# Performance work log

Hardware: AMD Instinct MI355X
Metric: run time of the kernel (lower is better)

## Reference

```python
import jax, jax.numpy as jnp
import numpy as np

N = 50000      # nodes
E = 500000     # edges (before self-loops)
IN = 128       # input feature dim
HID = 64       # hidden per head
HEADS = 8
OUT = 40       # classes
NEG_SLOPE = 0.2  # PyG GATConv default


def setup_inputs() -> dict:
    key = jax.random.key(0)
    ks = jax.random.split(key, 10)
    s = 0.05
    return {
        "x": jax.random.normal(ks[0], (N, IN), jnp.float32),
        "edge_index": jax.random.randint(ks[1], (2, E), 0, N, dtype=jnp.int32),
        "W1": jax.random.normal(ks[2], (IN, HEADS * HID), jnp.float32) * s,
        "a1_src": jax.random.normal(ks[3], (HEADS, HID), jnp.float32) * s,
        "a1_dst": jax.random.normal(ks[4], (HEADS, HID), jnp.float32) * s,
        "b1": jnp.zeros((HEADS * HID,), jnp.float32),
        "W2": jax.random.normal(ks[5], (HEADS * HID, OUT), jnp.float32) * s,
        "a2_src": jax.random.normal(ks[6], (1, OUT), jnp.float32) * s,
        "a2_dst": jax.random.normal(ks[7], (1, OUT), jnp.float32) * s,
        "b2": jnp.zeros((OUT,), jnp.float32),
    }


def gat_layer(x, src, dst, W, a_src, a_dst, b, heads, ch, concat):
    n = x.shape[0]
    h = (x @ W).reshape(n, heads, ch)                    # [N,H,C]
    e_src = jnp.einsum('nhc,hc->nh', h, a_src)           # [N,H]
    e_dst = jnp.einsum('nhc,hc->nh', h, a_dst)
    logits = jax.nn.leaky_relu(e_src[src] + e_dst[dst], NEG_SLOPE)  # [E,H]
    # segment softmax over incoming edges of each dst node
    m = jax.ops.segment_max(logits, dst, num_segments=n)
    p = jnp.exp(logits - m[dst])
    z = jax.ops.segment_sum(p, dst, num_segments=n)
    alpha = p / (z[dst] + 1e-16)                         # [E,H]
    out = jax.ops.segment_sum(h[src] * alpha[:, :, None], dst, num_segments=n)  # [N,H,C]
    out = out.reshape(n, heads * ch) if concat else out.mean(axis=1)
    return out + b


def reference(x, edge_index, W1, a1_src, a1_dst, b1, W2, a2_src, a2_dst, b2):
    loops = jnp.arange(N, dtype=edge_index.dtype)
    src = jnp.concatenate([edge_index[0], loops])        # add self-loops (PyG default)
    dst = jnp.concatenate([edge_index[1], loops])
    h = jax.nn.relu(gat_layer(x, src, dst, W1, a1_src, a1_dst, b1, HEADS, HID, True))
    h = gat_layer(h, src, dst, W2, a2_src, a2_dst, b2, 1, OUT, False)
    return jax.nn.log_softmax(h, axis=1)
```

## Files before the change

kernel.cpp:

```cpp
#include <hip/hip_runtime.h>
#include <math.h>

#define N_NODES 50000
#define E_EDGES 500000
#define E_TOT   550000
#define IN_DIM  128
#define HID     64
#define HEADS   8
#define HC      512
#define OUT_DIM 40
#define NEG_SLOPE 0.2f

__device__ __forceinline__ float leaky(float v){ return v > 0.f ? v : NEG_SLOPE * v; }


__global__ void k_hist(const int* __restrict__ ei, int* __restrict__ counts){
    int i = blockIdx.x * 256 + threadIdx.x;
    if (i < E_EDGES){
        atomicAdd(&counts[ei[E_EDGES + i]], 1);
    } else if (i < E_TOT){
        atomicAdd(&counts[i - E_EDGES], 1);
    }
}

__global__ void k_scanA(const int* __restrict__ counts, int* __restrict__ offsets,
                        int* __restrict__ blockSums){
    __shared__ int sh[1024];
    int b = blockIdx.x, t = threadIdx.x;
    int i = b * 1024 + t;
    int v = (i < N_NODES) ? counts[i] : 0;
    sh[t] = v; __syncthreads();
    for (int off = 1; off < 1024; off <<= 1){
        int add = (t >= off) ? sh[t - off] : 0;
        __syncthreads();
        sh[t] += add;
        __syncthreads();
    }
    if (i < N_NODES) offsets[i + 1] = sh[t];
    if (t == 1023) blockSums[b] = sh[t];
}

__global__ void k_scanB(int* __restrict__ blockSums, int nb){
    if (threadIdx.x == 0 && blockIdx.x == 0){
        int run = 0;
        for (int b = 0; b < nb; b++){ int v = blockSums[b]; blockSums[b] = run; run += v; }
    }
}

__global__ void k_scanC(const int* __restrict__ counts, int* __restrict__ offsets,
                        const int* __restrict__ blockSums, int* __restrict__ cursor){
    int b = blockIdx.x, t = threadIdx.x;
    int i = b * 1024 + t;
    if (i < N_NODES){
        int v = offsets[i + 1] + blockSums[b];
        offsets[i + 1] = v;
        cursor[i] = v - counts[i];
    }
    if (i == 0) offsets[0] = 0;
}

__global__ void k_scatter(const int* __restrict__ ei, int* __restrict__ cursor,
                          int* __restrict__ sortedSrc){
    int i = blockIdx.x * 256 + threadIdx.x;
    if (i < E_EDGES){
        int d = ei[E_EDGES + i];
        int pos = atomicAdd(&cursor[d], 1);
        sortedSrc[pos] = ei[i];
    } else if (i < E_TOT){
        int n = i - E_EDGES;
        int pos = atomicAdd(&cursor[n], 1);
        sortedSrc[pos] = n;
    }
}


__global__ __launch_bounds__(256) void k_gemm1e1(const float* __restrict__ x,
                                                 const float* __restrict__ W1,
                                                 const float* __restrict__ a1s,
                                                 const float* __restrict__ a1d,
                                                 float* __restrict__ h1,
                                                 float* __restrict__ e1s,
                                                 float* __restrict__ e1d){
    __shared__ float xs[16 * IN_DIM];
    const int t = threadIdx.x;
    const int row0 = blockIdx.x * 16;
    const float4* xg = (const float4*)(x + (size_t)row0 * IN_DIM);
    float4* xsv = (float4*)xs;
    xsv[t] = xg[t];
    xsv[t + 256] = xg[t + 256];
    __syncthreads();

    const int ct = t & 127;
    const int rg = t >> 7;
    float4 acc[8];
    #pragma unroll
    for (int r = 0; r < 8; r++) acc[r] = make_float4(0.f, 0.f, 0.f, 0.f);

    const float4* Wv = (const float4*)W1;
    for (int kb = 0; kb < IN_DIM; kb += 4){
        float4 w0 = Wv[(size_t)(kb + 0) * 128 + ct];
        float4 w1 = Wv[(size_t)(kb + 1) * 128 + ct];
        float4 w2 = Wv[(size_t)(kb + 2) * 128 + ct];
        float4 w3 = Wv[(size_t)(kb + 3) * 128 + ct];
        #pragma unroll
        for (int r = 0; r < 8; r++){
            float4 xv = *(const float4*)&xs[(rg * 8 + r) * IN_DIM + kb];
            acc[r].x = fmaf(xv.x, w0.x, acc[r].x); acc[r].y = fmaf(xv.x, w0.y, acc[r].y);
            acc[r].z = fmaf(xv.x, w0.z, acc[r].z); acc[r].w = fmaf(xv.x, w0.w, acc[r].w);
            acc[r].x = fmaf(xv.y, w1.x, acc[r].x); acc[r].y = fmaf(xv.y, w1.y, acc[r].y);
            acc[r].z = fmaf(xv.y, w1.z, acc[r].z); acc[r].w = fmaf(xv.y, w1.w, acc[r].w);
            acc[r].x = fmaf(xv.z, w2.x, acc[r].x); acc[r].y = fmaf(xv.z, w2.y, acc[r].y);
            acc[r].z = fmaf(xv.z, w2.z, acc[r].z); acc[r].w = fmaf(xv.z, w2.w, acc[r].w);
            acc[r].x = fmaf(xv.w, w3.x, acc[r].x); acc[r].y = fmaf(xv.w, w3.y, acc[r].y);
            acc[r].z = fmaf(xv.w, w3.z, acc[r].z); acc[r].w = fmaf(xv.w, w3.w, acc[r].w);
        }
    }

    const float4 as4 = ((const float4*)a1s)[ct];
    const float4 ad4 = ((const float4*)a1d)[ct];
    float4* h1v = (float4*)h1;
    float ps[8], pd[8];
    #pragma unroll
    for (int r = 0; r < 8; r++){
        int row = row0 + rg * 8 + r;
        h1v[(size_t)row * 128 + ct] = acc[r];
        ps[r] = acc[r].x * as4.x + acc[r].y * as4.y + acc[r].z * as4.z + acc[r].w * as4.w;
        pd[r] = acc[r].x * ad4.x + acc[r].y * ad4.y + acc[r].z * ad4.z + acc[r].w * ad4.w;
    }
    #pragma unroll
    for (int off = 1; off < 16; off <<= 1){
        #pragma unroll
        for (int r = 0; r < 8; r++){
            ps[r] += __shfl_xor(ps[r], off, 64);
            pd[r] += __shfl_xor(pd[r], off, 64);
        }
    }
    if ((t & 15) == 0){
        int h = (ct >> 4) & 7;
        #pragma unroll
        for (int r = 0; r < 8; r++){
            int row = row0 + rg * 8 + r;
            e1s[(size_t)row * HEADS + h] = ps[r];
            e1d[(size_t)row * HEADS + h] = pd[r];
        }
    }
}


__global__ __launch_bounds__(256) void k_agg1(const float* __restrict__ h1,
                                              const float* __restrict__ e1s,
                                              const float* __restrict__ e1d,
                                              const int* __restrict__ offsets,
                                              const int* __restrict__ sortedSrc,
                                              const float* __restrict__ b1,
                                              float* __restrict__ hmid){
    const int lane = threadIdx.x & 63;
    const int d = blockIdx.x * 4 + (threadIdx.x >> 6);
    if (d >= N_NODES) return;
    const int beg = offsets[d], end = offsets[d + 1];
    const int cnt = end - beg;
    const int h = lane >> 3;
    const int c0 = lane * 8;
    const float ed = e1d[(size_t)d * HEADS + h];

    float4 acc0 = make_float4(0.f,0.f,0.f,0.f), acc1 = make_float4(0.f,0.f,0.f,0.f);
    float z = 0.f;

    int s1 = 0, s2 = 0;
    float eA = 0.f; float4 hA0, hA1;
    {
        int s0 = sortedSrc[beg];
        eA = e1s[(size_t)s0 * HEADS + h];
        const float4* hp = (const float4*)(h1 + (size_t)s0 * HC + c0);
        hA0 = hp[0]; hA1 = hp[1];
        if (cnt > 1) s1 = sortedSrc[beg + 1];
    }
    for (int e = 0; e < cnt; ++e){
        if (e + 2 < cnt) s2 = sortedSrc[beg + e + 2];
        float eB = 0.f; float4 hB0, hB1;
        if (e + 1 < cnt){
            eB = e1s[(size_t)s1 * HEADS + h];
            const float4* hp = (const float4*)(h1 + (size_t)s1 * HC + c0);
            hB0 = hp[0]; hB1 = hp[1];
        }
        float w = __expf(leaky(eA + ed));
        z += w;
        acc0.x = fmaf(w, hA0.x, acc0.x); acc0.y = fmaf(w, hA0.y, acc0.y);
        acc0.z = fmaf(w, hA0.z, acc0.z); acc0.w = fmaf(w, hA0.w, acc0.w);
        acc1.x = fmaf(w, hA1.x, acc1.x); acc1.y = fmaf(w, hA1.y, acc1.y);
        acc1.z = fmaf(w, hA1.z, acc1.z); acc1.w = fmaf(w, hA1.w, acc1.w);
        eA = eB; hA0 = hB0; hA1 = hB1; s1 = s2;
    }

    const float inv = 1.f / (z + 1e-16f);
    const float4 bv0 = ((const float4*)b1)[lane * 2];
    const float4 bv1 = ((const float4*)b1)[lane * 2 + 1];
    float4 o0, o1;
    o0.x = fmaxf(fmaf(acc0.x, inv, bv0.x), 0.f);
    o0.y = fmaxf(fmaf(acc0.y, inv, bv0.y), 0.f);
    o0.z = fmaxf(fmaf(acc0.z, inv, bv0.z), 0.f);
    o0.w = fmaxf(fmaf(acc0.w, inv, bv0.w), 0.f);
    o1.x = fmaxf(fmaf(acc1.x, inv, bv1.x), 0.f);
    o1.y = fmaxf(fmaf(acc1.y, inv, bv1.y), 0.f);
    o1.z = fmaxf(fmaf(acc1.z, inv, bv1.z), 0.f);
    o1.w = fmaxf(fmaf(acc1.w, inv, bv1.w), 0.f);
    float4* op = (float4*)(hmid + (size_t)d * HC + c0);
    op[0] = o0; op[1] = o1;
}


__global__ __launch_bounds__(256) void k_gemm2e2(const float* __restrict__ hmid,
                                                 const float* __restrict__ W2,
                                                 const float* __restrict__ a2s,
                                                 const float* __restrict__ a2d,
                                                 float* __restrict__ h2,
                                                 float* __restrict__ e2s,
                                                 float* __restrict__ e2d){
    __shared__ float hs[64][64];
    __shared__ float ws[64 * OUT_DIM];
    const int t = threadIdx.x;
    const int row0 = blockIdx.x * 64;
    const int col = t & 63;
    const int rbase = t >> 6;
    float acc[16];
    #pragma unroll
    for (int i = 0; i < 16; i++) acc[i] = 0.f;

    for (int kb = 0; kb < HC; kb += 64){
        for (int i = t; i < 64 * 64; i += 256){
            int r = i >> 6, k = i & 63;
            int gr = row0 + r;
            hs[r][k] = (gr < N_NODES) ? hmid[(size_t)gr * HC + kb + k] : 0.f;
        }
        for (int i = t; i < 64 * OUT_DIM; i += 256){
            int k = i / OUT_DIM, j = i - k * OUT_DIM;
            ws[i] = W2[(size_t)(kb + k) * OUT_DIM + j];
        }
        __syncthreads();
        if (col < OUT_DIM){
            for (int k = 0; k < 64; k++){
                float w = ws[k * OUT_DIM + col];
                #pragma unroll
                for (int i = 0; i < 16; i++)
                    acc[i] = fmaf(hs[rbase + 4 * i][k], w, acc[i]);
            }
        }
        __syncthreads();
    }

    const float as = (col < OUT_DIM) ? a2s[col] : 0.f;
    const float ad = (col < OUT_DIM) ? a2d[col] : 0.f;
    #pragma unroll
    for (int i = 0; i < 16; i++){
        int r = row0 + rbase + 4 * i;
        bool ok = (col < OUT_DIM) && (r < N_NODES);
        float v = ok ? acc[i] : 0.f;
        if (ok) h2[(size_t)r * OUT_DIM + col] = v;
        float pvs = v * as, pvd = v * ad;
        #pragma unroll
        for (int off = 32; off > 0; off >>= 1){
            pvs += __shfl_xor(pvs, off, 64);
            pvd += __shfl_xor(pvd, off, 64);
        }
        if (col == 0 && r < N_NODES){ e2s[r] = pvs; e2d[r] = pvd; }
    }
}


__global__ __launch_bounds__(256) void k_agg2(const float* __restrict__ h2,
                                              const float* __restrict__ e2s,
                                              const float* __restrict__ e2d,
                                              const int* __restrict__ offsets,
                                              const int* __restrict__ sortedSrc,
                                              const float* __restrict__ b2,
                                              float* __restrict__ out){
    const int lane = threadIdx.x & 63;
    const int d = blockIdx.x * 4 + (threadIdx.x >> 6);
    if (d >= N_NODES) return;
    const int beg = offsets[d], end = offsets[d + 1];
    const int cnt = end - beg;
    const float ed = e2d[d];
    const bool act = (lane < OUT_DIM);

    float acc = 0.f, z = 0.f;
    int s1 = 0, s2 = 0;
    float eA = 0.f, hA = 0.f;
    {
        int s0 = sortedSrc[beg];
        eA = e2s[s0];
        if (act) hA = h2[(size_t)s0 * OUT_DIM + lane];
        if (cnt > 1) s1 = sortedSrc[beg + 1];
    }
    for (int e = 0; e < cnt; ++e){
        if (e + 2 < cnt) s2 = sortedSrc[beg + e + 2];
        float eB = 0.f, hB = 0.f;
        if (e + 1 < cnt){
            eB = e2s[s1];
            if (act) hB = h2[(size_t)s1 * OUT_DIM + lane];
        }
        float w = __expf(leaky(eA + ed));
        z += w;
        acc = fmaf(w, hA, acc);
        eA = eB; hA = hB; s1 = s2;
    }

    float o = acc / (z + 1e-16f) + (act ? b2[lane] : 0.f);
    float ov = act ? o : -INFINITY;
    float vmax = ov;
    #pragma unroll
    for (int off = 32; off > 0; off >>= 1) vmax = fmaxf(vmax, __shfl_xor(vmax, off, 64));
    float se = act ? __expf(o - vmax) : 0.f;
    #pragma unroll
    for (int off = 32; off > 0; off >>= 1) se += __shfl_xor(se, off, 64);
    if (act) out[(size_t)d * OUT_DIM + lane] = o - vmax - __logf(se);
}


extern "C" void kernel_launch(void* const* d_in, const int* in_sizes, int n_in,
                              void* d_out, int out_size, void* d_ws, size_t ws_size,
                              hipStream_t stream){
    const float* x   = (const float*)d_in[0];
    const int*   ei  = (const int*)  d_in[1];
    const float* W1  = (const float*)d_in[2];
    const float* a1s = (const float*)d_in[3];
    const float* a1d = (const float*)d_in[4];
    const float* b1  = (const float*)d_in[5];
    const float* W2  = (const float*)d_in[6];
    const float* a2s = (const float*)d_in[7];
    const float* a2d = (const float*)d_in[8];
    const float* b2  = (const float*)d_in[9];
    float* out = (float*)d_out;

    char* ws = (char*)d_ws;
    size_t off = 0;
    auto alloc = [&](size_t bytes) -> char* {
        off = (off + 255) & ~(size_t)255;
        char* p = ws + off;
        off += bytes;
        return p;
    };

    float* h1      = (float*)alloc((size_t)N_NODES * HC * 4);
    float* hmid    = (float*)alloc((size_t)N_NODES * HC * 4);
    float* h2      = (float*)alloc((size_t)N_NODES * OUT_DIM * 4);
    float* e1s     = (float*)alloc((size_t)N_NODES * HEADS * 4);
    float* e1d     = (float*)alloc((size_t)N_NODES * HEADS * 4);
    float* e2s     = (float*)alloc((size_t)N_NODES * 4);
    float* e2d     = (float*)alloc((size_t)N_NODES * 4);
    int* counts    = (int*)alloc((size_t)N_NODES * 4);
    int* offsets   = (int*)alloc((size_t)(N_NODES + 1) * 4);
    int* cursor    = (int*)alloc((size_t)N_NODES * 4);
    int* blockSums = (int*)alloc(64 * 4);
    int* sortedSrc = (int*)alloc((size_t)E_TOT * 4);

    const int nb = (N_NODES + 1023) / 1024;

    hipMemsetAsync(counts, 0, (size_t)N_NODES * 4, stream);
    k_hist   <<<(E_TOT + 255) / 256, 256, 0, stream>>>(ei, counts);
    k_scanA  <<<nb, 1024, 0, stream>>>(counts, offsets, blockSums);
    k_scanB  <<<1, 64, 0, stream>>>(blockSums, nb);
    k_scanC  <<<nb, 1024, 0, stream>>>(counts, offsets, blockSums, cursor);
    k_scatter<<<(E_TOT + 255) / 256, 256, 0, stream>>>(ei, cursor, sortedSrc);

    k_gemm1e1<<<N_NODES / 16, 256, 0, stream>>>(x, W1, a1s, a1d, h1, e1s, e1d);
    k_agg1   <<<(N_NODES + 3) / 4, 256, 0, stream>>>(h1, e1s, e1d, offsets, sortedSrc, b1, hmid);

    k_gemm2e2<<<(N_NODES + 63) / 64, 256, 0, stream>>>(hmid, W2, a2s, a2d, h2, e2s, e2d);
    k_agg2   <<<(N_NODES + 3) / 4, 256, 0, stream>>>(h2, e2s, e2d, offsets, sortedSrc, b2, out);
}
```

Baseline: 644.1 us.

## Register-block the second-layer GEMM with 4x5 per-thread tiles

The layer-2 GEMM kernel is rewritten so each thread computes a 4-row by 5-column output tile instead of 16 rows of one column. The old version left 24 of every 64 lanes idle. Each block now covers 128 rows with a 32-wide K tile, loads hmid with float4, and stores padded, transposed W2 in shared memory so the inner loop can read float2 values. The attention-score reduction shrinks to a 3-step shuffle across 8 lanes. This raises arithmetic intensity and removes idle lanes, at the cost of more registers and possible LDS bank conflicts.

```diff
diff --git a/kernel.cpp b/kernel.cpp
--- a/kernel.cpp
+++ b/kernel.cpp
@@ -216,53 +216,71 @@
                                                  float* __restrict__ h2,
                                                  float* __restrict__ e2s,
                                                  float* __restrict__ e2d){
-    __shared__ float hs[64][64];
-    __shared__ float ws[64 * OUT_DIM];
+    __shared__ float hs[128][34];
+    __shared__ float ws[OUT_DIM][34];
     const int t = threadIdx.x;
-    const int row0 = blockIdx.x * 64;
-    const int col = t & 63;
-    const int rbase = t >> 6;
-    float acc[16];
-    #pragma unroll
-    for (int i = 0; i < 16; i++) acc[i] = 0.f;
-
-    for (int kb = 0; kb < HC; kb += 64){
-        for (int i = t; i < 64 * 64; i += 256){
-            int r = i >> 6, k = i & 63;
+    const int row0 = blockIdx.x * 128;
+    const int tc = t & 7;
+    const int tr = t >> 3;
+
+    float acc[4][5];
+    #pragma unroll
+    for (int i = 0; i < 4; i++)
+        #pragma unroll
+        for (int j = 0; j < 5; j++) acc[i][j] = 0.f;
+
+    for (int kb = 0; kb < HC; kb += 32){
+        #pragma unroll
+        for (int p = 0; p < 4; p++){
+            int q = t + 256 * p;
+            int r = q >> 3, k4 = (q & 7) * 4;
             int gr = row0 + r;
-            hs[r][k] = (gr < N_NODES) ? hmid[(size_t)gr * HC + kb + k] : 0.f;
-        }
-        for (int i = t; i < 64 * OUT_DIM; i += 256){
+            float4 v = (gr < N_NODES) ? *(const float4*)&hmid[(size_t)gr * HC + kb + k4]
+                                      : make_float4(0.f, 0.f, 0.f, 0.f);
+            *(float2*)&hs[r][k4]     = make_float2(v.x, v.y);
+            *(float2*)&hs[r][k4 + 2] = make_float2(v.z, v.w);
+        }
+        for (int i = t; i < 32 * OUT_DIM; i += 256){
             int k = i / OUT_DIM, j = i - k * OUT_DIM;
-            ws[i] = W2[(size_t)(kb + k) * OUT_DIM + j];
+            ws[j][k] = W2[(size_t)(kb + k) * OUT_DIM + j];
         }
         __syncthreads();
-        if (col < OUT_DIM){
-            for (int k = 0; k < 64; k++){
-                float w = ws[k * OUT_DIM + col];
+        #pragma unroll
+        for (int k = 0; k < 32; k += 2){
+            float2 hv[4], wv[5];
+            #pragma unroll
+            for (int i = 0; i < 4; i++) hv[i] = *(const float2*)&hs[tr * 4 + i][k];
+            #pragma unroll
+            for (int j = 0; j < 5; j++) wv[j] = *(const float2*)&ws[tc * 5 + j][k];
+            #pragma unroll
+            for (int i = 0; i < 4; i++)
                 #pragma unroll
-                for (int i = 0; i < 16; i++)
-                    acc[i] = fmaf(hs[rbase + 4 * i][k], w, acc[i]);
-            }
+                for (int j = 0; j < 5; j++){
+                    acc[i][j] = fmaf(hv[i].x, wv[j].x, acc[i][j]);
+                    acc[i][j] = fmaf(hv[i].y, wv[j].y, acc[i][j]);
+                }
         }
         __syncthreads();
     }
 
-    const float as = (col < OUT_DIM) ? a2s[col] : 0.f;
-    const float ad = (col < OUT_DIM) ? a2d[col] : 0.f;
-    #pragma unroll
-    for (int i = 0; i < 16; i++){
-        int r = row0 + rbase + 4 * i;
-        bool ok = (col < OUT_DIM) && (r < N_NODES);
-        float v = ok ? acc[i] : 0.f;
-        if (ok) h2[(size_t)r * OUT_DIM + col] = v;
-        float pvs = v * as, pvd = v * ad;
-        #pragma unroll
-        for (int off = 32; off > 0; off >>= 1){
-            pvs += __shfl_xor(pvs, off, 64);
-            pvd += __shfl_xor(pvd, off, 64);
-        }
-        if (col == 0 && r < N_NODES){ e2s[r] = pvs; e2d[r] = pvd; }
+    float as[5], ad[5];
+    #pragma unroll
+    for (int j = 0; j < 5; j++){ as[j] = a2s[tc * 5 + j]; ad[j] = a2d[tc * 5 + j]; }
+    #pragma unroll
+    for (int i = 0; i < 4; i++){
+        int r = row0 + tr * 4 + i;
+        bool ok = (r < N_NODES);
+        float pvs = 0.f, pvd = 0.f;
+        #pragma unroll
+        for (int j = 0; j < 5; j++){
+            if (ok) h2[(size_t)r * OUT_DIM + tc * 5 + j] = acc[i][j];
+            pvs = fmaf(acc[i][j], as[j], pvs);
+            pvd = fmaf(acc[i][j], ad[j], pvd);
+        }
+        pvs += __shfl_xor(pvs, 1, 64); pvd += __shfl_xor(pvd, 1, 64);
+        pvs += __shfl_xor(pvs, 2, 64); pvd += __shfl_xor(pvd, 2, 64);
+        pvs += __shfl_xor(pvs, 4, 64); pvd += __shfl_xor(pvd, 4, 64);
+        if (tc == 0 && ok){ e2s[r] = pvs; e2d[r] = pvd; }
     }
 }
 
@@ -365,6 +383,6 @@
     k_gemm1e1<<<N_NODES / 16, 256, 0, stream>>>(x, W1, a1s, a1d, h1, e1s, e1d);
     k_agg1   <<<(N_NODES + 3) / 4, 256, 0, stream>>>(h1, e1s, e1d, offsets, sortedSrc, b1, hmid);
 
-    k_gemm2e2<<<(N_NODES + 63) / 64, 256, 0, stream>>>(hmid, W2, a2s, a2d, h2, e2s, e2d);
+    k_gemm2e2<<<(N_NODES + 127) / 128, 256, 0, stream>>>(hmid, W2, a2s, a2d, h2, e2s, e2d);
     k_agg2   <<<(N_NODES + 3) / 4, 256, 0, stream>>>(h2, e2s, e2d, offsets, sortedSrc, b2, out);
 }
```

Result: faster. 560.3 us (-13.0%).
